# Kernel optimization log

Measured on AMD Instinct MI355X. Metric: run time of the kernel, lower is better.

Reference implementation:

```python
import jax, jax.numpy as jnp
import numpy as np

N, E, D, H, C = 50000, 1600000, 128, 2, 32

def setup_inputs() -> dict:
    key = jax.random.key(0)
    ks = jax.random.split(key, 8)
    x = jax.random.normal(ks[0], (N, D), jnp.float32)
    edge_index = jax.random.randint(ks[1], (2, E), 0, N)
    intra_enrichment_weights = jax.random.uniform(ks[2], (E,), jnp.float32)
    W = jax.random.normal(ks[3], (D, H * C), jnp.float32) * (1.0 / np.sqrt(D))
    att_src = jax.random.normal(ks[4], (H, C), jnp.float32) * 0.1
    att_dst = jax.random.normal(ks[5], (H, C), jnp.float32) * 0.1
    bias = jnp.zeros((H * C,), jnp.float32)
    enrichment_scale = jnp.asarray(0.01, jnp.float32)
    return dict(x=x, edge_index=edge_index,
                intra_enrichment_weights=intra_enrichment_weights,
                W=W, att_src=att_src, att_dst=att_dst, bias=bias,
                enrichment_scale=enrichment_scale)

def reference(x, edge_index, intra_enrichment_weights, W, att_src, att_dst, bias, enrichment_scale):
    n = x.shape[0]
    xf = jax.nn.elu(x)                       # F.elu on input features
    h = (xf @ W).reshape(n, H, C)            # [N, heads, out]
    # GATConv default add_self_loops=True
    loop = jnp.arange(n, dtype=edge_index.dtype)
    src = jnp.concatenate([edge_index[0], loop])
    dst = jnp.concatenate([edge_index[1], loop])
    a_src = jnp.einsum('nhc,hc->nh', h, att_src)   # [N, H]
    a_dst = jnp.einsum('nhc,hc->nh', h, att_dst)
    alpha = jax.nn.leaky_relu(a_src[src] + a_dst[dst], 0.2)  # [E+N, H]
    # softmax over incoming edges per destination node
    m = jax.ops.segment_max(alpha, dst, num_segments=n)
    e = jnp.exp(alpha - m[dst])
    denom = jax.ops.segment_sum(e, dst, num_segments=n)
    p = e / denom[dst]                       # every node has a self-loop -> denom > 0
    out = jax.ops.segment_sum(h[src] * p[:, :, None], dst, num_segments=n)  # [N, H, C]
    out = out.reshape(n, H * C) + bias
    # enrichment bias (scatter-mean of per-edge weights over source nodes)
    s0 = edge_index[0]
    nw = jax.ops.segment_sum(intra_enrichment_weights, s0, num_segments=n)
    cnt = jax.ops.segment_sum(jnp.ones_like(intra_enrichment_weights), s0, num_segments=n)
    nw = nw / jnp.maximum(cnt, 1.0)
    nw = jnp.clip(nw, 0.2, 5.0)
    scale_factor = 0.1 * jax.nn.sigmoid(enrichment_scale)
    return out + scale_factor * (nw[:, None] - 1.0)
```

## Files before the change

### kernel.cpp

```cpp
#include <hip/hip_runtime.h>


typedef unsigned int u32;
typedef unsigned short u16;

#define SLOTS 4864
#define NB_MAX 400
#define EPB 4096

#define XS 136
#define CS 68

typedef __attribute__((ext_vector_type(8))) short short8;
typedef __attribute__((ext_vector_type(4))) float float4v;

__device__ __forceinline__ u16 f2bf(float f) {
    union { float f; u32 u; } v; v.f = f;
    u32 r = v.u + 0x7fffu + ((v.u >> 16) & 1u);
    return (u16)(r >> 16);
}
__device__ __forceinline__ float bf2f(u16 u) {
    union { u32 i; float f; } v; v.i = ((u32)u) << 16; return v.f;
}
__device__ __forceinline__ float bf_lo(u32 u) {
    union { u32 i; float f; } v; v.i = u << 16; return v.f;
}
__device__ __forceinline__ float bf_hi(u32 u) {
    union { u32 i; float f; } v; v.i = u & 0xFFFF0000u; return v.f;
}
__device__ __forceinline__ void bf_split(float v, short& hi, short& lo) {
    u16 h = f2bf(v);
    float hf = bf2f(h);
    hi = (short)h;
    lo = (short)f2bf(v - hf);
}

__global__ void k_init(int* cursA, int* cursB, int nb) {
    int t = threadIdx.x;
    if (t < nb) { cursA[t] = 0; cursB[t] = 0; }
}

__global__ __launch_bounds__(256) void k_node(
    const float* __restrict__ x, const float* __restrict__ Wm,
    const float* __restrict__ att_s, const float* __restrict__ att_d,
    u32* __restrict__ hb32, float* __restrict__ a_src, float* __restrict__ a_dst,
    int nN)
{
    __shared__ __align__(16) short Ah[64 * XS];
    __shared__ __align__(16) short Al[64 * XS];
    __shared__ __align__(16) short Bh[64 * XS];
    __shared__ __align__(16) short Bl[64 * XS];
    float* Cl = (float*)Ah;

    int t = threadIdx.x;
    int n0 = blockIdx.x * 64;

    {
        int f = t & 63, kq = t >> 6;
        for (int kk = 0; kk < 32; ++kk) {
            int k = kq * 32 + kk;
            float wv = Wm[k * 64 + f];
            short hi, lo; bf_split(wv, hi, lo);
            Bh[f * XS + k] = hi; Bl[f * XS + k] = lo;
        }
    }
    for (int j = 0; j < 8; ++j) {
        int idx = t + 256 * j;
        int r = idx >> 5, c4 = idx & 31;
        int gn = n0 + r;
        float4 xv = make_float4(0.f, 0.f, 0.f, 0.f);
        if (gn < nN) xv = ((const float4*)x)[(size_t)gn * 32 + c4];
        float e[4];
        e[0] = xv.x > 0.f ? xv.x : expm1f(xv.x);
        e[1] = xv.y > 0.f ? xv.y : expm1f(xv.y);
        e[2] = xv.z > 0.f ? xv.z : expm1f(xv.z);
        e[3] = xv.w > 0.f ? xv.w : expm1f(xv.w);
        short h4[4], l4[4];
#pragma unroll
        for (int i = 0; i < 4; ++i) bf_split(e[i], h4[i], l4[i]);
        *(short4*)&Ah[r * XS + c4 * 4] = make_short4(h4[0], h4[1], h4[2], h4[3]);
        *(short4*)&Al[r * XS + c4 * 4] = make_short4(l4[0], l4[1], l4[2], l4[3]);
    }
    __syncthreads();

    {
        int w = t >> 6, l = t & 63;
        int q = l >> 4, m = l & 15;
        int arow = w * 16 + m;
        float4v acc[4] = {};
#pragma unroll
        for (int ks = 0; ks < 4; ++ks) {
            int k0 = ks * 32 + q * 8;
            short8 ah = *(const short8*)&Ah[arow * XS + k0];
            short8 al = *(const short8*)&Al[arow * XS + k0];
#pragma unroll
            for (int nt = 0; nt < 4; ++nt) {
                short8 bh = *(const short8*)&Bh[(nt * 16 + m) * XS + k0];
                short8 bl = *(const short8*)&Bl[(nt * 16 + m) * XS + k0];
                acc[nt] = __builtin_amdgcn_mfma_f32_16x16x32_bf16(ah, bh, acc[nt], 0, 0, 0);
                acc[nt] = __builtin_amdgcn_mfma_f32_16x16x32_bf16(ah, bl, acc[nt], 0, 0, 0);
                acc[nt] = __builtin_amdgcn_mfma_f32_16x16x32_bf16(al, bh, acc[nt], 0, 0, 0);
            }
        }
        __syncthreads();
#pragma unroll
        for (int nt = 0; nt < 4; ++nt)
#pragma unroll
            for (int r = 0; r < 4; ++r)
                Cl[(w * 16 + q * 4 + r) * CS + nt * 16 + m] = acc[nt][r];
    }
    __syncthreads();

    {
        int nl = t >> 2, fq = t & 3;
        int gn = n0 + nl;
        float ps = 0.f, pd = 0.f;
        if (gn < nN) {
            float hv[16];
#pragma unroll
            for (int i = 0; i < 16; ++i) {
                int f = fq * 16 + i;
                hv[i] = Cl[nl * CS + f];
                ps = fmaf(hv[i], att_s[f], ps);
                pd = fmaf(hv[i], att_d[f], pd);
            }
#pragma unroll
            for (int i = 0; i < 8; ++i) {
                u32 pk = ((u32)f2bf(hv[2 * i + 1]) << 16) | (u32)f2bf(hv[2 * i]);
                hb32[(size_t)gn * 32 + fq * 8 + i] = pk;
            }
        }
        float ps2 = ps + __shfl_xor(ps, 1, 64);
        float pd2 = pd + __shfl_xor(pd, 1, 64);
        if (gn < nN && (fq & 1) == 0) {
            a_src[2 * gn + (fq >> 1)] = ps2;
            a_dst[2 * gn + (fq >> 1)] = pd2;
        }
    }
}

__global__ __launch_bounds__(256) void k_partA(
    const int* __restrict__ ei, const float* __restrict__ wgt,
    int* cursA, int* cursB, u32* bufA, u32* bufB, int E, int nb)
{
    __shared__ u32 arrA[EPB], arrB[EPB];
    __shared__ u16 bkA[EPB], bkB[EPB];
    __shared__ int cntA[NB_MAX], cntB[NB_MAX];
    __shared__ int lofsA[NB_MAX], lofsB[NB_MAX];
    __shared__ int basA[NB_MAX], basB[NB_MAX];
    __shared__ int part[256];

    int t = threadIdx.x;
    for (int b = t; b < nb; b += 256) { cntA[b] = 0; cntB[b] = 0; }
    __syncthreads();

    int base = blockIdx.x * EPB;
    int nv = min(EPB, E - base);
    int sv[16], dv[16]; float wv[16];
#pragma unroll
    for (int k = 0; k < 16; ++k) {
        int e = base + k * 256 + t;
        if (e < E) { sv[k] = ei[e]; dv[k] = ei[E + e]; wv[k] = wgt[e]; }
        else       { sv[k] = -1;    dv[k] = -1;        wv[k] = 0.f; }
    }
#pragma unroll
    for (int k = 0; k < 16; ++k) {
        if (dv[k] >= 0) {
            atomicAdd(&cntA[dv[k] >> 7], 1);
            atomicAdd(&cntB[sv[k] >> 7], 1);
        }
    }
    __syncthreads();
    for (int b = t; b < nb; b += 256) {
        int ca = cntA[b], cb = cntB[b];
        if (ca > 0) basA[b] = atomicAdd(&cursA[b], ca);
        if (cb > 0) basB[b] = atomicAdd(&cursB[b], cb);
    }
    __syncthreads();
    {
        int b0 = 2 * t, b1 = 2 * t + 1;
        int c0 = (b0 < nb) ? cntA[b0] : 0;
        int c1 = (b1 < nb) ? cntA[b1] : 0;
        part[t] = c0 + c1;
        __syncthreads();
        for (int off = 1; off < 256; off <<= 1) {
            int v = (t >= off) ? part[t - off] : 0;
            __syncthreads();
            part[t] += v;
            __syncthreads();
        }
        int excl = part[t] - (c0 + c1);
        if (b0 < nb) lofsA[b0] = excl;
        if (b1 < nb) lofsA[b1] = excl + c0;
        __syncthreads();
        c0 = (b0 < nb) ? cntB[b0] : 0;
        c1 = (b1 < nb) ? cntB[b1] : 0;
        part[t] = c0 + c1;
        __syncthreads();
        for (int off = 1; off < 256; off <<= 1) {
            int v = (t >= off) ? part[t - off] : 0;
            __syncthreads();
            part[t] += v;
            __syncthreads();
        }
        excl = part[t] - (c0 + c1);
        if (b0 < nb) lofsB[b0] = excl;
        if (b1 < nb) lofsB[b1] = excl + c0;
    }
    __syncthreads();
    for (int b = t; b < nb; b += 256) { cntA[b] = 0; cntB[b] = 0; }
    __syncthreads();
#pragma unroll
    for (int k = 0; k < 16; ++k) {
        if (dv[k] >= 0) {
            int bA = dv[k] >> 7;
            int r = lofsA[bA] + atomicAdd(&cntA[bA], 1);
            arrA[r] = ((u32)(dv[k] & 127) << 16) | (u32)sv[k];
            bkA[r] = (u16)bA;
            int bB = sv[k] >> 7;
            u32 wf = (u32)(wv[k] * 16777216.f);
            if (wf > 0xFFFFFFu) wf = 0xFFFFFFu;
            int r2 = lofsB[bB] + atomicAdd(&cntB[bB], 1);
            arrB[r2] = ((u32)(sv[k] & 127) << 24) | wf;
            bkB[r2] = (u16)bB;
        }
    }
    __syncthreads();
    for (int i = t; i < nv; i += 256) {
        int bA = bkA[i];
        int g = basA[bA] + (i - lofsA[bA]);
        if (g < SLOTS) bufA[bA * SLOTS + g] = arrA[i];
    }
    for (int i = t; i < nv; i += 256) {
        int bB = bkB[i];
        int g = basB[bB] + (i - lofsB[bB]);
        if (g < SLOTS) bufB[bB * SLOTS + g] = arrB[i];
    }
}

__global__ __launch_bounds__(256) void k_partB(
    const u32* bufA_in, const int* __restrict__ cursA,
    u32* bufA_out, int* __restrict__ deg, int* __restrict__ offs,
    const u32* __restrict__ bufB, const int* __restrict__ cursB,
    float* __restrict__ nwv, int nN)
{
    __shared__ u32 st[SLOTS];
    __shared__ u32 st2[SLOTS];
    __shared__ int ldeg[128], lscan[128], lcur[128];
    __shared__ u32 usum[128]; __shared__ int ucnt[128];
    int b = blockIdx.x, t = threadIdx.x;
    int nA = cursA[b]; if (nA > SLOTS) nA = SLOTS;
    int nB = cursB[b]; if (nB > SLOTS) nB = SLOTS;
    if (t < 128) { ldeg[t] = 0; lcur[t] = 0; usum[t] = 0; ucnt[t] = 0; }
    __syncthreads();
    for (int i = t; i < nA; i += 256) {
        u32 v = bufA_in[b * SLOTS + i];
        st[i] = v;
        atomicAdd(&ldeg[v >> 16], 1);
    }
    for (int i = t; i < nB; i += 256) {
        u32 v = bufB[b * SLOTS + i];
        atomicAdd(&usum[v >> 24], v & 0xFFFFFFu);
        atomicAdd(&ucnt[v >> 24], 1);
    }
    __syncthreads();
    if (t < 128) lscan[t] = ldeg[t];
    __syncthreads();
    for (int off = 1; off < 128; off <<= 1) {
        int v = 0;
        if (t < 128 && t >= off) v = lscan[t - off];
        __syncthreads();
        if (t < 128) lscan[t] += v;
        __syncthreads();
    }
    int excl = 0;
    if (t < 128) excl = lscan[t] - ldeg[t];
    __syncthreads();
    if (t < 128) lscan[t] = excl;
    __syncthreads();
    for (int i = t; i < nA; i += 256) {
        u32 v = st[i];
        int dl = v >> 16;
        int pos = lscan[dl] + atomicAdd(&lcur[dl], 1);
        st2[pos] = v & 0xFFFFu;
    }
    __syncthreads();
    for (int i = t; i < nA; i += 256) bufA_out[b * SLOTS + i] = st2[i];
    int node = (b << 7) + t;
    if (t < 128 && node < nN) {
        deg[node] = ldeg[t];
        offs[node] = b * SLOTS + lscan[t];
        float cnt = (float)ucnt[t];
        float nw = ((float)usum[t] * (1.f / 16777216.f)) / fmaxf(cnt, 1.f);
        nwv[node] = fminf(fmaxf(nw, 0.2f), 5.f);
    }
}

__global__ __launch_bounds__(256) void k_accum(
    const u32* __restrict__ hb32,
    const float* __restrict__ a_src, const float* __restrict__ a_dst,
    const u32* __restrict__ esrc, const int* __restrict__ offs,
    const int* __restrict__ deg, const float* __restrict__ nwv,
    const float* __restrict__ bias, const float* __restrict__ esc,
    float* __restrict__ out, int nN)
{
    __shared__ u32    lds_si[4][64];
    __shared__ float2 lds_w[4][64];
    int tid = threadIdx.x;
    int lane = tid & 63;
    int n = (blockIdx.x * 256 + tid) >> 6;
    if (n >= nN) return;
    int ws = tid >> 6;
    int q  = lane >> 4;
    int fl = lane & 15;
    int head = fl >> 3;

    float ad0 = a_dst[2 * n], ad1 = a_dst[2 * n + 1];
    float as0 = a_src[2 * n], as1 = a_src[2 * n + 1];
    float t0 = as0 + ad0; t0 = t0 > 0.f ? t0 : 0.2f * t0;
    float t1 = as1 + ad1; t1 = t1 > 0.f ? t1 : 0.2f * t1;
    float es0 = __expf(t0), es1 = __expf(t1);

    const uint2* hb2 = (const uint2*)hb32;
    float acc0 = 0.f, acc1 = 0.f, acc2 = 0.f, acc3 = 0.f;
    if (q == 0) {
        uint2 hs = hb2[(size_t)n * 16 + fl];
        float eself = head ? es1 : es0;
        acc0 = eself * bf_lo(hs.x);
        acc1 = eself * bf_hi(hs.x);
        acc2 = eself * bf_lo(hs.y);
        acc3 = eself * bf_hi(hs.y);
    }
    float dsum0 = 0.f, dsum1 = 0.f;

    int start = offs[n], len = deg[n];
    for (int b0 = 0; b0 < len; b0 += 64) {
        int cnt = min(64, len - b0);
        u32 si = (u32)n; float e0 = 0.f, e1 = 0.f;
        if (lane < cnt) {
            si = esrc[start + b0 + lane];
            float2 ap = ((const float2*)a_src)[si];
            float v0 = ap.x + ad0; v0 = v0 > 0.f ? v0 : 0.2f * v0;
            float v1 = ap.y + ad1; v1 = v1 > 0.f ? v1 : 0.2f * v1;
            e0 = __expf(v0); e1 = __expf(v1);
        }
        dsum0 += e0; dsum1 += e1;
        lds_si[ws][lane] = si;
        lds_w[ws][lane]  = make_float2(e0, e1);

        int iters = (cnt + 3) >> 2;
#pragma unroll 8
        for (int k = 0; k < iters; ++k) {
            int e = 4 * k + q;
            u32 rsi = lds_si[ws][e];
            float2 w2 = lds_w[ws][e];
            float w = head ? w2.y : w2.x;
            uint2 hv = hb2[(size_t)rsi * 16 + fl];
            acc0 = fmaf(w, bf_lo(hv.x), acc0);
            acc1 = fmaf(w, bf_hi(hv.x), acc1);
            acc2 = fmaf(w, bf_lo(hv.y), acc2);
            acc3 = fmaf(w, bf_hi(hv.y), acc3);
        }
    }

#pragma unroll
    for (int off = 1; off < 64; off <<= 1) {
        dsum0 += __shfl_xor(dsum0, off, 64);
        dsum1 += __shfl_xor(dsum1, off, 64);
    }
    float den0 = es0 + dsum0, den1 = es1 + dsum1;

    acc0 += __shfl_xor(acc0, 16, 64); acc0 += __shfl_xor(acc0, 32, 64);
    acc1 += __shfl_xor(acc1, 16, 64); acc1 += __shfl_xor(acc1, 32, 64);
    acc2 += __shfl_xor(acc2, 16, 64); acc2 += __shfl_xor(acc2, 32, 64);
    acc3 += __shfl_xor(acc3, 16, 64); acc3 += __shfl_xor(acc3, 32, 64);

    if (q == 0) {
        float den = head ? den1 : den0;
        float sf = 0.1f / (1.f + __expf(-esc[0]));
        float en = sf * (nwv[n] - 1.f);
        float4 bb = ((const float4*)bias)[fl];
        float4 o;
        o.x = acc0 / den + bb.x + en;
        o.y = acc1 / den + bb.y + en;
        o.z = acc2 / den + bb.z + en;
        o.w = acc3 / den + bb.w + en;
        ((float4*)out)[(size_t)n * 16 + fl] = o;
    }
}

extern "C" void kernel_launch(void* const* d_in, const int* in_sizes, int n_in,
                              void* d_out, int out_size, void* d_ws, size_t ws_size,
                              hipStream_t stream)
{
    const float* x     = (const float*)d_in[0];
    const int*   ei    = (const int*)d_in[1];
    const float* wgt   = (const float*)d_in[2];
    const float* Wm    = (const float*)d_in[3];
    const float* att_s = (const float*)d_in[4];
    const float* att_d = (const float*)d_in[5];
    const float* bias  = (const float*)d_in[6];
    const float* esc   = (const float*)d_in[7];
    float* out = (float*)d_out;

    int nN = in_sizes[0] / 128;
    int E  = in_sizes[2];
    int NB = (nN + 127) / 128;

    char* p = (char*)d_ws;
    auto alloc = [&](size_t bytes) -> char* {
        char* r = p; p += (bytes + 255) & ~(size_t)255; return r;
    };
    u32*   hb32  = (u32*)  alloc((size_t)nN * 32 * 4);
    float* a_src = (float*)alloc((size_t)nN * 2 * 4);
    float* a_dst = (float*)alloc((size_t)nN * 2 * 4);
    int*   deg   = (int*)  alloc((size_t)nN * 4);
    int*   offs  = (int*)  alloc((size_t)nN * 4);
    float* nwv   = (float*)alloc((size_t)nN * 4);
    int*   cursA = (int*)  alloc(NB_MAX * 4);
    int*   cursB = (int*)  alloc(NB_MAX * 4);
    u32*   bufA  = (u32*)  alloc((size_t)NB * SLOTS * 4);
    u32*   bufB  = (u32*)  alloc((size_t)NB * SLOTS * 4);

    int nblkA = (E + EPB - 1) / EPB;

    k_init<<<dim3(1), dim3(512), 0, stream>>>(cursA, cursB, NB);
    k_node<<<dim3((nN + 63) / 64), dim3(256), 0, stream>>>(x, Wm, att_s, att_d, hb32, a_src, a_dst, nN);
    k_partA<<<dim3(nblkA), dim3(256), 0, stream>>>(ei, wgt, cursA, cursB, bufA, bufB, E, NB);
    k_partB<<<dim3(NB), dim3(256), 0, stream>>>(bufA, cursA, bufA, deg, offs, bufB, cursB, nwv, nN);
    k_accum<<<dim3((nN + 3) / 4), dim3(256), 0, stream>>>(hb32, a_src, a_dst, bufA, offs, deg,
                                                          nwv, bias, esc, out, nN);
}
```

Measured before the change: 190.6 us.

## Fuse node transform and edge partition into one interleaved kernel; shuffle edge weights

```diff
diff --git a/kernel.cpp b/kernel.cpp
--- a/kernel.cpp
+++ b/kernel.cpp
@@ -10,6 +10,8 @@
 
 #define XS 136
 #define CS 68
+
+#define SMEM_BYTES 69632
 
 typedef __attribute__((ext_vector_type(8))) short short8;
 typedef __attribute__((ext_vector_type(4))) float float4v;
@@ -35,25 +37,21 @@
     lo = (short)f2bf(v - hf);
 }
 
-__global__ void k_init(int* cursA, int* cursB, int nb) {
-    int t = threadIdx.x;
-    if (t < nb) { cursA[t] = 0; cursB[t] = 0; }
-}
-
-__global__ __launch_bounds__(256) void k_node(
+static __device__ __forceinline__ void node_body(
+    char* smem, int nb_id,
     const float* __restrict__ x, const float* __restrict__ Wm,
     const float* __restrict__ att_s, const float* __restrict__ att_d,
     u32* __restrict__ hb32, float* __restrict__ a_src, float* __restrict__ a_dst,
     int nN)
 {
-    __shared__ __align__(16) short Ah[64 * XS];
-    __shared__ __align__(16) short Al[64 * XS];
-    __shared__ __align__(16) short Bh[64 * XS];
-    __shared__ __align__(16) short Bl[64 * XS];
+    short* Ah = (short*)smem;
+    short* Al = (short*)(smem + 17408);
+    short* Bh = (short*)(smem + 34816);
+    short* Bl = (short*)(smem + 52224);
     float* Cl = (float*)Ah;
 
     int t = threadIdx.x;
-    int n0 = blockIdx.x * 64;
+    int n0 = nb_id * 64;
 
     {
         int f = t & 63, kq = t >> 6;
@@ -139,22 +137,28 @@
     }
 }
 
-__global__ __launch_bounds__(256) void k_partA(
+static __device__ __forceinline__ void partA_body(
+    char* smem, int pa_id,
     const int* __restrict__ ei, const float* __restrict__ wgt,
     int* cursA, int* cursB, u32* bufA, u32* bufB, int E, int nb)
 {
-    __shared__ u32 arrA[EPB], arrB[EPB];
-    __shared__ u16 bkA[EPB], bkB[EPB];
-    __shared__ int cntA[NB_MAX], cntB[NB_MAX];
-    __shared__ int lofsA[NB_MAX], lofsB[NB_MAX];
-    __shared__ int basA[NB_MAX], basB[NB_MAX];
-    __shared__ int part[256];
+    u32* arrA  = (u32*)smem;
+    u32* arrB  = (u32*)(smem + 16384);
+    u16* bkA   = (u16*)(smem + 32768);
+    u16* bkB   = (u16*)(smem + 40960);
+    int* cntA  = (int*)(smem + 49152);
+    int* cntB  = (int*)(smem + 50752);
+    int* lofsA = (int*)(smem + 52352);
+    int* lofsB = (int*)(smem + 53952);
+    int* basA  = (int*)(smem + 55552);
+    int* basB  = (int*)(smem + 57152);
+    int* part  = (int*)(smem + 58752);
 
     int t = threadIdx.x;
     for (int b = t; b < nb; b += 256) { cntA[b] = 0; cntB[b] = 0; }
     __syncthreads();
 
-    int base = blockIdx.x * EPB;
+    int base = pa_id * EPB;
     int nv = min(EPB, E - base);
     int sv[16], dv[16]; float wv[16];
 #pragma unroll
@@ -238,6 +242,25 @@
     }
 }
 
+__global__ __launch_bounds__(256) void k_fused(
+    const float* __restrict__ x, const float* __restrict__ Wm,
+    const float* __restrict__ att_s, const float* __restrict__ att_d,
+    u32* __restrict__ hb32, float* __restrict__ a_src, float* __restrict__ a_dst,
+    const int* __restrict__ ei, const float* __restrict__ wgt,
+    int* cursA, int* cursB, u32* bufA, u32* bufB,
+    int E, int nb, int nblkA, int nN)
+{
+    __shared__ __align__(16) char smem[SMEM_BYTES];
+    int bid = blockIdx.x;
+    int q3 = bid / 3;
+    if ((bid % 3) == 0 && q3 < nblkA) {
+        partA_body(smem, q3, ei, wgt, cursA, cursB, bufA, bufB, E, nb);
+    } else {
+        int npa_before = min(q3 + ((bid % 3) ? 1 : 0), nblkA);
+        node_body(smem, bid - npa_before, x, Wm, att_s, att_d, hb32, a_src, a_dst, nN);
+    }
+}
+
 __global__ __launch_bounds__(256) void k_partB(
     const u32* bufA_in, const int* __restrict__ cursA,
     u32* bufA_out, int* __restrict__ deg, int* __restrict__ offs,
@@ -304,19 +327,21 @@
     const float* __restrict__ bias, const float* __restrict__ esc,
     float* __restrict__ out, int nN)
 {
-    __shared__ u32    lds_si[4][64];
-    __shared__ float2 lds_w[4][64];
     int tid = threadIdx.x;
     int lane = tid & 63;
     int n = (blockIdx.x * 256 + tid) >> 6;
     if (n >= nN) return;
-    int ws = tid >> 6;
     int q  = lane >> 4;
     int fl = lane & 15;
     int head = fl >> 3;
 
     float ad0 = a_dst[2 * n], ad1 = a_dst[2 * n + 1];
     float as0 = a_src[2 * n], as1 = a_src[2 * n + 1];
+    int start = offs[n], len = deg[n];
+    float nw = nwv[n];
+    float escv = esc[0];
+    float4 bb = ((const float4*)bias)[fl];
+
     float t0 = as0 + ad0; t0 = t0 > 0.f ? t0 : 0.2f * t0;
     float t1 = as1 + ad1; t1 = t1 > 0.f ? t1 : 0.2f * t1;
     float es0 = __expf(t0), es1 = __expf(t1);
@@ -333,29 +358,28 @@
     }
     float dsum0 = 0.f, dsum1 = 0.f;
 
-    int start = offs[n], len = deg[n];
     for (int b0 = 0; b0 < len; b0 += 64) {
         int cnt = min(64, len - b0);
-        u32 si = (u32)n; float e0 = 0.f, e1 = 0.f;
+        u32 si = (u32)n;
+        if (lane < cnt) si = esrc[start + b0 + lane];
+        float2 ap = ((const float2*)a_src)[si];
+        float e0 = 0.f, e1 = 0.f;
         if (lane < cnt) {
-            si = esrc[start + b0 + lane];
-            float2 ap = ((const float2*)a_src)[si];
             float v0 = ap.x + ad0; v0 = v0 > 0.f ? v0 : 0.2f * v0;
             float v1 = ap.y + ad1; v1 = v1 > 0.f ? v1 : 0.2f * v1;
             e0 = __expf(v0); e1 = __expf(v1);
         }
         dsum0 += e0; dsum1 += e1;
-        lds_si[ws][lane] = si;
-        lds_w[ws][lane]  = make_float2(e0, e1);
 
         int iters = (cnt + 3) >> 2;
 #pragma unroll 8
         for (int k = 0; k < iters; ++k) {
             int e = 4 * k + q;
-            u32 rsi = lds_si[ws][e];
-            float2 w2 = lds_w[ws][e];
-            float w = head ? w2.y : w2.x;
+            u32 rsi = __shfl(si, e, 64);
             uint2 hv = hb2[(size_t)rsi * 16 + fl];
+            float w0 = __shfl(e0, e, 64);
+            float w1 = __shfl(e1, e, 64);
+            float w = head ? w1 : w0;
             acc0 = fmaf(w, bf_lo(hv.x), acc0);
             acc1 = fmaf(w, bf_hi(hv.x), acc1);
             acc2 = fmaf(w, bf_lo(hv.y), acc2);
@@ -377,9 +401,8 @@
 
     if (q == 0) {
         float den = head ? den1 : den0;
-        float sf = 0.1f / (1.f + __expf(-esc[0]));
-        float en = sf * (nwv[n] - 1.f);
-        float4 bb = ((const float4*)bias)[fl];
+        float sf = 0.1f / (1.f + __expf(-escv));
+        float en = sf * (nw - 1.f);
         float4 o;
         o.x = acc0 / den + bb.x + en;
         o.y = acc1 / den + bb.y + en;
@@ -423,10 +446,13 @@
     u32*   bufB  = (u32*)  alloc((size_t)NB * SLOTS * 4);
 
     int nblkA = (E + EPB - 1) / EPB;
-
-    k_init<<<dim3(1), dim3(512), 0, stream>>>(cursA, cursB, NB);
-    k_node<<<dim3((nN + 63) / 64), dim3(256), 0, stream>>>(x, Wm, att_s, att_d, hb32, a_src, a_dst, nN);
-    k_partA<<<dim3(nblkA), dim3(256), 0, stream>>>(ei, wgt, cursA, cursB, bufA, bufB, E, NB);
+    int nblkN = (nN + 63) / 64;
+    int nblkF = nblkA + nblkN;
+
+    hipMemsetAsync(cursA, 0, (size_t)((char*)bufA - (char*)cursA), stream);
+    k_fused<<<dim3(nblkF), dim3(256), 0, stream>>>(x, Wm, att_s, att_d, hb32, a_src, a_dst,
+                                                   ei, wgt, cursA, cursB, bufA, bufB,
+                                                   E, NB, nblkA, nN);
     k_partB<<<dim3(NB), dim3(256), 0, stream>>>(bufA, cursA, bufA, deg, offs, bufB, cursB, nwv, nN);
     k_accum<<<dim3((nN + 3) / 4), dim3(256), 0, stream>>>(hb32, a_src, a_dst, bufA, offs, deg,
                                                           nwv, bias, esc, out, nN);
```

New measurement: 189.3 us. Within noise of the previous version (-0.7%).
